# Kernel tuning notes

Hardware: AMD Instinct MI355X
Metric: run time of the kernel (lower is better)

The kernel has to match this reference:

```python
import jax, jax.numpy as jnp
import numpy as np

H = 128      # hidden_channels
FN = 6       # in_channels_node
FE = 3       # in_channels_edge
N = 40000    # nodes per chunk (pointnum)
E = 240000   # edges
C = 2        # per_t * batch_size chunks
S = 4        # n_mp_down[0] message-passing steps


def _ln(x, g, b, eps=1e-5):
    m = jnp.mean(x, axis=-1, keepdims=True)
    v = jnp.mean((x - m) ** 2, axis=-1, keepdims=True)
    return (x - m) * jax.lax.rsqrt(v + eps) * g + b


def setup_inputs() -> dict:
    key = jax.random.key(0)
    ks = iter(jax.random.split(key, 64))
    def W(*shape):
        fan_in = shape[-2]
        return jax.random.normal(next(ks), shape, jnp.float32) * (1.0 / np.sqrt(fan_in))
    z = lambda *s: jnp.zeros(s, jnp.float32)
    o = lambda *s: jnp.ones(s, jnp.float32)
    inp = {
        "x": jax.random.normal(next(ks), (C * N, FN), jnp.float32),
        "edge_attr": jax.random.normal(next(ks), (E, FE), jnp.float32),
        "mean_vec_x": jax.random.normal(next(ks), (FN,), jnp.float32) * 0.1,
        "std_vec_x": o(FN),
        "mean_vec_edge": jax.random.normal(next(ks), (FE,), jnp.float32) * 0.1,
        "std_vec_edge": o(FE),
        # node encoder: 3 linears + LayerNorm
        "nenc_w0": W(FN, H), "nenc_b0": z(H),
        "nenc_w1": W(H, H), "nenc_b1": z(H),
        "nenc_w2": W(H, H), "nenc_b2": z(H),
        "nenc_g": o(H), "nenc_be": z(H),
        # edge encoder: 3 linears + LayerNorm
        "eenc_w0": W(FE, H), "eenc_b0": z(H),
        "eenc_w1": W(H, H), "eenc_b1": z(H),
        "eenc_w2": W(H, H), "eenc_b2": z(H),
        "eenc_g": o(H), "eenc_be": z(H),
        # per-step edge MLPs (n_mlp_mp=2), stacked over S steps
        "emp_w0": W(S, 3 * H, H), "emp_b0": z(S, H),
        "emp_w1": W(S, H, H), "emp_b1": z(S, H),
        "emp_g": o(S, H), "emp_be": z(S, H),
        # per-step node MLPs
        "nmp_w0": W(S, 2 * H, H), "nmp_b0": z(S, H),
        "nmp_w1": W(S, H, H), "nmp_b1": z(S, H),
        "nmp_g": o(S, H), "nmp_be": z(S, H),
        "edge_index": jax.random.randint(next(ks), (2, E), 0, N, jnp.int32),
        "per_t": 2,
        "batch_size": 1,
    }
    return inp


def _forward(x, edge_attr, mean_vec_x, std_vec_x, mean_vec_edge, std_vec_edge,
             nenc_w0, nenc_b0, nenc_w1, nenc_b1, nenc_w2, nenc_b2, nenc_g, nenc_be,
             eenc_w0, eenc_b0, eenc_w1, eenc_b1, eenc_w2, eenc_b2, eenc_g, eenc_be,
             emp_w0, emp_b0, emp_w1, emp_b1, emp_g, emp_be,
             nmp_w0, nmp_b0, nmp_w1, nmp_b1, nmp_g, nmp_be,
             edge_index, per_t, batch_size):
    act = jax.nn.elu
    ei0, ei1 = edge_index[0], edge_index[1]
    chunks = per_t * batch_size
    n = x.shape[0] // chunks  # pointnum
    # edge encoding is identical for every chunk (shared edge_attr)
    e = (edge_attr - mean_vec_edge) / std_vec_edge
    e = act(e @ eenc_w0 + eenc_b0)
    e = act(e @ eenc_w1 + eenc_b1)
    e = e @ eenc_w2 + eenc_b2
    e0 = _ln(e, eenc_g, eenc_be)
    # scatter-mean denominator (PyG aggr='mean' at target nodes ei1)
    cnt = jax.ops.segment_sum(jnp.ones((ei1.shape[0], 1), x.dtype), ei1, num_segments=n)
    cnt = jnp.maximum(cnt, 1.0)

    def chunk(xc):  # xc: [n, FN]
        h = (xc - mean_vec_x) / std_vec_x
        h = act(h @ nenc_w0 + nenc_b0)
        h = act(h @ nenc_w1 + nenc_b1)
        h = h @ nenc_w2 + nenc_b2
        h = _ln(h, nenc_g, nenc_be)
        e = e0
        for s in range(S):
            # per-edge: gather -> concat -> 2-layer MLP -> residual -> LN
            et = jnp.concatenate([h[ei0], h[ei1], e], axis=-1)  # [E, 3H]
            et = act(et @ emp_w0[s] + emp_b0[s]) @ emp_w1[s] + emp_b1[s]
            e = _ln(e + et, emp_g[s], emp_be[s])
            # scatter-mean of edge features to target nodes
            agg = jax.ops.segment_sum(e, ei1, num_segments=n) / cnt  # [n, H]
            # per-node: concat -> 2-layer MLP -> residual -> LN
            ht = jnp.concatenate([h, agg], axis=-1)  # [n, 2H]
            ht = act(ht @ nmp_w0[s] + nmp_b0[s]) @ nmp_w1[s] + nmp_b1[s]
            h = _ln(h + ht, nmp_g[s], nmp_be[s])
        return h

    return jax.vmap(chunk)(x.reshape(chunks, n, FN))  # [C, n, H]


def reference(x, edge_attr, mean_vec_x, std_vec_x, mean_vec_edge, std_vec_edge,
              nenc_w0, nenc_b0, nenc_w1, nenc_b1, nenc_w2, nenc_b2, nenc_g, nenc_be,
              eenc_w0, eenc_b0, eenc_w1, eenc_b1, eenc_w2, eenc_b2, eenc_g, eenc_be,
              emp_w0, emp_b0, emp_w1, emp_b1, emp_g, emp_be,
              nmp_w0, nmp_b0, nmp_w1, nmp_b1, nmp_g, nmp_be,
              edge_index, per_t, batch_size):
    return _forward(x, edge_attr, mean_vec_x, std_vec_x, mean_vec_edge, std_vec_edge,
                    nenc_w0, nenc_b0, nenc_w1, nenc_b1, nenc_w2, nenc_b2, nenc_g, nenc_be,
                    eenc_w0, eenc_b0, eenc_w1, eenc_b1, eenc_w2, eenc_b2, eenc_g, eenc_be,
                    emp_w0, emp_b0, emp_w1, emp_b1, emp_g, emp_be,
                    nmp_w0, nmp_b0, nmp_w1, nmp_b1, nmp_g, nmp_be,
                    edge_index, per_t, batch_size)
```

## Files before the change

### kernel.cpp

```cpp
#include <hip/hip_runtime.h>
#include <math.h>

constexpr int HD  = 128;
constexpr int FNN = 6;
constexpr int FEE = 3;
constexpr int NN  = 40000;
constexpr int EE  = 240000;
constexpr int SS  = 4;

typedef __bf16 bf16_t;
typedef bf16_t bf16x8 __attribute__((ext_vector_type(8)));
typedef float  f32x4  __attribute__((ext_vector_type(4)));

__device__ __forceinline__ f32x4 mfma16(bf16x8 a, bf16x8 b, f32x4 c){
  return __builtin_amdgcn_mfma_f32_16x16x32_bf16(a, b, c, 0, 0, 0);
}
__device__ __forceinline__ float elu(float v){ return v > 0.f ? v : __expf(v) - 1.f; }

struct PackJob { const float* src; int K; };
struct PackArgs { PackJob j[30]; };

__global__ void __launch_bounds__(256) k_pack(PackArgs pa, bf16_t* __restrict__ dst){
  int gid = blockIdx.x*256 + threadIdx.x;
  int base = 0;
  #pragma unroll 1
  for (int i = 0; i < 30; ++i){
    int Kp = (pa.j[i].K + 31) & ~31;
    int sz = Kp * HD;
    if (gid < base + sz){
      int idx = gid - base;
      int jj = idx & 7, c = (idx >> 3) & 127, G = idx >> 10;
      int k = G*8 + jj;
      float v = (k < pa.j[i].K) ? pa.j[i].src[(size_t)k*HD + c] : 0.f;
      dst[base + idx] = (bf16_t)v;
      return;
    }
    base += sz;
  }
}

__global__ void k_cnt(const int* __restrict__ ei1, int* __restrict__ cnt){
  int t = blockIdx.x*blockDim.x + threadIdx.x;
  if (t < EE) atomicAdd(cnt + ei1[t], 1);
}

__global__ void __launch_bounds__(1024) k_scan(const int* __restrict__ cnt,
    int* __restrict__ rowstart, int* __restrict__ cursor, float* __restrict__ inv){
  __shared__ int sdata[1024];
  __shared__ int carry_s;
  if (threadIdx.x == 0) carry_s = 0;
  __syncthreads();
  for (int base = 0; base < NN; base += 1024){
    int i = base + (int)threadIdx.x;
    int orig = (i < NN) ? cnt[i] : 0;
    sdata[threadIdx.x] = orig;
    __syncthreads();
    #pragma unroll
    for (int ofs = 1; ofs < 1024; ofs <<= 1){
      int t = (threadIdx.x >= (unsigned)ofs) ? sdata[threadIdx.x - ofs] : 0;
      __syncthreads();
      sdata[threadIdx.x] += t;
      __syncthreads();
    }
    int incl = sdata[threadIdx.x];
    int carry = carry_s;
    if (i < NN){
      int start = carry + incl - orig;
      rowstart[i] = start;
      cursor[i]   = start;
      inv[i] = 1.f / fmaxf((float)orig, 1.f);
    }
    __syncthreads();
    if (threadIdx.x == 1023) carry_s = carry + incl;
    __syncthreads();
  }
  if (threadIdx.x == 0) rowstart[NN] = carry_s;
}

__global__ void k_fill(const int* __restrict__ ei0, const int* __restrict__ ei1,
                       int* __restrict__ cursor, int* __restrict__ perm,
                       int2* __restrict__ eidx2){
  int t = blockIdx.x*blockDim.x + threadIdx.x;
  if (t < EE){
    int n1 = ei1[t];
    int pos = atomicAdd(cursor + n1, 1);
    perm[pos] = t;
    int2 v; v.x = ei0[t]; v.y = n1;
    eidx2[pos] = v;
  }
}

__global__ void __launch_bounds__(256) k_agg(const bf16_t* __restrict__ e,
    const int* __restrict__ rowstart, const float* __restrict__ inv,
    bf16_t* __restrict__ agg){
  int gid = blockIdx.x*256 + (int)threadIdx.x;
  int node = gid >> 4, li = gid & 15;
  if (node >= NN) return;
  int s = rowstart[node], t = rowstart[node+1];
  float a[8] = {0,0,0,0,0,0,0,0};
  for (int ed = s; ed < t; ++ed){
    bf16x8 v = *(const bf16x8*)(e + (size_t)ed*HD + li*8);
    #pragma unroll
    for (int i = 0; i < 8; ++i) a[i] += (float)v[i];
  }
  float sc = inv[node];
  bf16x8 o;
  #pragma unroll
  for (int i = 0; i < 8; ++i) o[i] = (bf16_t)(a[i]*sc);
  *(bf16x8*)(agg + (size_t)node*HD + li*8) = o;
}

template<int FIN, bool ISNODE>
__global__ void __launch_bounds__(256) k_encoder(
    const float* __restrict__ xin, const float* __restrict__ mv, const float* __restrict__ sv,
    const float* __restrict__ w0,  const float* __restrict__ b0,
    const bf16_t* __restrict__ W1p, const float* __restrict__ b1,
    const bf16_t* __restrict__ W2p, const float* __restrict__ b2,
    const float* __restrict__ gg,  const float* __restrict__ bb,
    float* __restrict__ outf, bf16_t* __restrict__ outb,
    const int* __restrict__ perm)
{
  __shared__ bf16_t z0s[4][16][136];
  __shared__ bf16_t z1s[4][16][136];
  const int tid = threadIdx.x;
  const int w = tid >> 6, l = tid & 63, r = l & 15, grp = l >> 4;
  const int rowbase = blockIdx.x*64 + w*16;
  const int row = rowbase + r;
  const int src = perm ? perm[row] : row;

  float xn[FIN];
  #pragma unroll
  for (int f = 0; f < FIN; ++f) xn[f] = (xin[(size_t)src*FIN + f] - mv[f]) / sv[f];
  #pragma unroll
  for (int q = 0; q < 32; ++q){
    int c = grp*32 + q;
    float a = b0[c];
    #pragma unroll
    for (int f = 0; f < FIN; ++f) a += xn[f] * w0[f*HD + c];
    z0s[w][r][c] = (bf16_t)elu(a);
  }
  __syncthreads();

  bf16x8 a1[4];
  #pragma unroll
  for (int kt = 0; kt < 4; ++kt) a1[kt] = *(const bf16x8*)&z0s[w][r][kt*32 + grp*8];
  #pragma unroll
  for (int nt = 0; nt < 8; ++nt){
    int c = nt*16 + r;
    float bv = b1[c];
    f32x4 acc = {bv, bv, bv, bv};
    #pragma unroll
    for (int kt = 0; kt < 4; ++kt){
      bf16x8 bfr = *(const bf16x8*)(W1p + ((kt*4 + grp)*HD + c)*8);
      acc = mfma16(a1[kt], bfr, acc);
    }
    #pragma unroll
    for (int i = 0; i < 4; ++i) z1s[w][grp*4 + i][c] = (bf16_t)elu(acc[i]);
  }
  __syncthreads();

  bf16x8 a2[4];
  #pragma unroll
  for (int kt = 0; kt < 4; ++kt) a2[kt] = *(const bf16x8*)&z1s[w][r][kt*32 + grp*8];
  f32x4 et[8];
  #pragma unroll
  for (int nt = 0; nt < 8; ++nt){
    int c = nt*16 + r;
    float bv = b2[c];
    f32x4 acc = {bv, bv, bv, bv};
    #pragma unroll
    for (int kt = 0; kt < 4; ++kt){
      bf16x8 bfr = *(const bf16x8*)(W2p + ((kt*4 + grp)*HD + c)*8);
      acc = mfma16(a2[kt], bfr, acc);
    }
    et[nt] = acc;
  }

  f32x4 s = {0,0,0,0}, sq = {0,0,0,0};
  #pragma unroll
  for (int nt = 0; nt < 8; ++nt)
    #pragma unroll
    for (int i = 0; i < 4; ++i){ float v = et[nt][i]; s[i] += v; sq[i] += v*v; }
  #pragma unroll
  for (int m = 1; m < 16; m <<= 1)
    #pragma unroll
    for (int i = 0; i < 4; ++i){ s[i] += __shfl_xor(s[i], m, 64); sq[i] += __shfl_xor(sq[i], m, 64); }
  f32x4 mean, rstd;
  #pragma unroll
  for (int i = 0; i < 4; ++i){
    float mu = s[i] * (1.f/HD);
    float va = sq[i] * (1.f/HD) - mu*mu;
    mean[i] = mu; rstd[i] = rsqrtf(va + 1e-5f);
  }
  #pragma unroll
  for (int nt = 0; nt < 8; ++nt){
    int c = nt*16 + r;
    float gv = gg[c], bv = bb[c];
    #pragma unroll
    for (int i = 0; i < 4; ++i){
      float o = (et[nt][i] - mean[i]) * rstd[i] * gv + bv;
      size_t oidx = (size_t)(rowbase + grp*4 + i)*HD + c;
      outb[oidx] = (bf16_t)o;
      if constexpr (ISNODE) outf[oidx] = o;
    }
  }
}

__global__ void __launch_bounds__(256) k_hpartial(
    const bf16_t* __restrict__ hbf,
    const bf16_t* __restrict__ Wap, const bf16_t* __restrict__ Wbp,
    bf16_t* __restrict__ p0, bf16_t* __restrict__ p1)
{
  const int tid = threadIdx.x;
  const int w = tid >> 6, l = tid & 63, r = l & 15, grp = l >> 4;
  const int rowbase = blockIdx.x*64 + w*16;
  const int row = rowbase + r;

  bf16x8 afr[4];
  #pragma unroll
  for (int kt = 0; kt < 4; ++kt)
    afr[kt] = *(const bf16x8*)(hbf + (size_t)row*HD + kt*32 + grp*8);

  #pragma unroll
  for (int nt = 0; nt < 8; ++nt){
    int c = nt*16 + r;
    f32x4 a0 = {0,0,0,0}, a1 = {0,0,0,0};
    #pragma unroll
    for (int kt = 0; kt < 4; ++kt){
      bf16x8 bfa = *(const bf16x8*)(Wap + ((kt*4 + grp)*HD + c)*8);
      bf16x8 bfb = *(const bf16x8*)(Wbp + ((kt*4 + grp)*HD + c)*8);
      a0 = mfma16(afr[kt], bfa, a0);
      a1 = mfma16(afr[kt], bfb, a1);
    }
    #pragma unroll
    for (int i = 0; i < 4; ++i){
      size_t oidx = (size_t)(rowbase + grp*4 + i)*HD + c;
      p0[oidx] = (bf16_t)a0[i];
      p1[oidx] = (bf16_t)a1[i];
    }
  }
}

__global__ void __launch_bounds__(256) k_edge_mlp(
    const bf16_t* __restrict__ p0g, const bf16_t* __restrict__ p1g,
    const bf16_t* e_in, bf16_t* e_out,
    const bf16_t* __restrict__ W0ep, const float* __restrict__ b0,
    const bf16_t* __restrict__ W1p, const float* __restrict__ b1,
    const float* __restrict__ gg,  const float* __restrict__ bb,
    const int2* __restrict__ eidx2)
{
  __shared__ bf16_t z1s_all[4][16][136];
  const int tid = threadIdx.x;
  const int w = tid >> 6, l = tid & 63, r = l & 15, grp = l >> 4;
  const int rowbase = blockIdx.x*64 + w*16;
  const int row = rowbase + r;
  bf16_t (*z1)[136] = z1s_all[w];

  {
    const int sr = l >> 2, cq = (l & 3)*32;
    const int2 nnS = eidx2[rowbase + sr];
    const bf16_t* P0 = p0g + (size_t)nnS.x*HD + cq;
    const bf16_t* P1 = p1g + (size_t)nnS.y*HD + cq;
    #pragma unroll
    for (int q = 0; q < 4; ++q){
      bf16x8 u = *(const bf16x8*)(P0 + q*8);
      bf16x8 v = *(const bf16x8*)(P1 + q*8);
      bf16x8 sm;
      #pragma unroll
      for (int i = 0; i < 8; ++i) sm[i] = (bf16_t)((float)u[i] + (float)v[i]);
      *(bf16x8*)&z1[sr][cq + q*8] = sm;
    }
  }

  bf16x8 afr[4];
  #pragma unroll
  for (int kt = 0; kt < 4; ++kt)
    afr[kt] = *(const bf16x8*)(e_in + (size_t)row*HD + kt*32 + grp*8);
  __builtin_amdgcn_wave_barrier();

  #pragma unroll
  for (int nt = 0; nt < 8; ++nt){
    int c = nt*16 + r;
    float bv = b0[c];
    f32x4 acc = {bv, bv, bv, bv};
    #pragma unroll
    for (int kt = 0; kt < 4; ++kt){
      bf16x8 bfr = *(const bf16x8*)(W0ep + ((kt*4 + grp)*HD + c)*8);
      acc = mfma16(afr[kt], bfr, acc);
    }
    #pragma unroll
    for (int i = 0; i < 4; ++i){
      float pv = (float)z1[grp*4 + i][c];
      z1[grp*4 + i][c] = (bf16_t)elu(acc[i] + pv);
    }
  }
  __builtin_amdgcn_wave_barrier();

  bf16x8 a2[4];
  #pragma unroll
  for (int kt = 0; kt < 4; ++kt) a2[kt] = *(const bf16x8*)&z1[r][kt*32 + grp*8];
  f32x4 et[8];
  #pragma unroll
  for (int nt = 0; nt < 8; ++nt){
    int c = nt*16 + r;
    float bv = b1[c];
    f32x4 acc = {bv, bv, bv, bv};
    #pragma unroll
    for (int kt = 0; kt < 4; ++kt){
      bf16x8 bfr = *(const bf16x8*)(W1p + ((kt*4 + grp)*HD + c)*8);
      acc = mfma16(a2[kt], bfr, acc);
    }
    et[nt] = acc;
  }

  f32x4 s = {0,0,0,0}, sq = {0,0,0,0};
  #pragma unroll
  for (int nt = 0; nt < 8; ++nt){
    int c = nt*16 + r;
    #pragma unroll
    for (int i = 0; i < 4; ++i){
      float v = et[nt][i] + (float)e_in[(size_t)(rowbase + grp*4 + i)*HD + c];
      et[nt][i] = v; s[i] += v; sq[i] += v*v;
    }
  }
  #pragma unroll
  for (int m = 1; m < 16; m <<= 1)
    #pragma unroll
    for (int i = 0; i < 4; ++i){ s[i] += __shfl_xor(s[i], m, 64); sq[i] += __shfl_xor(sq[i], m, 64); }
  f32x4 mean, rstd;
  #pragma unroll
  for (int i = 0; i < 4; ++i){
    float mu = s[i] * (1.f/HD);
    float va = sq[i] * (1.f/HD) - mu*mu;
    mean[i] = mu; rstd[i] = rsqrtf(va + 1e-5f);
  }
  #pragma unroll
  for (int nt = 0; nt < 8; ++nt){
    int c = nt*16 + r;
    float gv = gg[c], bv = bb[c];
    #pragma unroll
    for (int i = 0; i < 4; ++i)
      e_out[(size_t)(rowbase + grp*4 + i)*HD + c] =
          (bf16_t)((et[nt][i] - mean[i]) * rstd[i] * gv + bv);
  }
}

__global__ void __launch_bounds__(256) k_node_mlp(
    bf16_t* hbf, const bf16_t* __restrict__ agg,
    const bf16_t* __restrict__ W0p, const float* __restrict__ b0,
    const bf16_t* __restrict__ W1p, const float* __restrict__ b1,
    const float* __restrict__ gg,  const float* __restrict__ bb,
    float* hout)
{
  __shared__ bf16_t z1s[4][16][136];
  const int tid = threadIdx.x;
  const int w = tid >> 6, l = tid & 63, r = l & 15, grp = l >> 4;
  const int rowbase = blockIdx.x*64 + w*16;
  const int row = rowbase + r;

  bf16x8 afr[8];
  #pragma unroll
  for (int kt = 0; kt < 4; ++kt)
    afr[kt] = *(const bf16x8*)(hbf + (size_t)row*HD + kt*32 + grp*8);
  #pragma unroll
  for (int kt = 0; kt < 4; ++kt)
    afr[4+kt] = *(const bf16x8*)(agg + (size_t)row*HD + kt*32 + grp*8);

  #pragma unroll
  for (int nt = 0; nt < 8; ++nt){
    int c = nt*16 + r;
    float bv = b0[c];
    f32x4 acc = {bv, bv, bv, bv};
    #pragma unroll
    for (int kt = 0; kt < 8; ++kt){
      bf16x8 bfr = *(const bf16x8*)(W0p + ((kt*4 + grp)*HD + c)*8);
      acc = mfma16(afr[kt], bfr, acc);
    }
    #pragma unroll
    for (int i = 0; i < 4; ++i) z1s[w][grp*4 + i][c] = (bf16_t)elu(acc[i]);
  }
  __syncthreads();

  bf16x8 a2[4];
  #pragma unroll
  for (int kt = 0; kt < 4; ++kt) a2[kt] = *(const bf16x8*)&z1s[w][r][kt*32 + grp*8];
  f32x4 et[8];
  #pragma unroll
  for (int nt = 0; nt < 8; ++nt){
    int c = nt*16 + r;
    float bv = b1[c];
    f32x4 acc = {bv, bv, bv, bv};
    #pragma unroll
    for (int kt = 0; kt < 4; ++kt){
      bf16x8 bfr = *(const bf16x8*)(W1p + ((kt*4 + grp)*HD + c)*8);
      acc = mfma16(a2[kt], bfr, acc);
    }
    et[nt] = acc;
  }

  f32x4 s = {0,0,0,0}, sq = {0,0,0,0};
  #pragma unroll
  for (int nt = 0; nt < 8; ++nt){
    int c = nt*16 + r;
    #pragma unroll
    for (int i = 0; i < 4; ++i){
      float v = et[nt][i] + hout[(size_t)(rowbase + grp*4 + i)*HD + c];
      et[nt][i] = v; s[i] += v; sq[i] += v*v;
    }
  }
  #pragma unroll
  for (int m = 1; m < 16; m <<= 1)
    #pragma unroll
    for (int i = 0; i < 4; ++i){ s[i] += __shfl_xor(s[i], m, 64); sq[i] += __shfl_xor(sq[i], m, 64); }
  f32x4 mean, rstd;
  #pragma unroll
  for (int i = 0; i < 4; ++i){
    float mu = s[i] * (1.f/HD);
    float va = sq[i] * (1.f/HD) - mu*mu;
    mean[i] = mu; rstd[i] = rsqrtf(va + 1e-5f);
  }
  #pragma unroll
  for (int nt = 0; nt < 8; ++nt){
    int c = nt*16 + r;
    float gv = gg[c], bv = bb[c];
    #pragma unroll
    for (int i = 0; i < 4; ++i){
      float o = (et[nt][i] - mean[i]) * rstd[i] * gv + bv;
      size_t oidx = (size_t)(rowbase + grp*4 + i)*HD + c;
      hout[oidx] = o;
      hbf[oidx]  = (bf16_t)o;
    }
  }
}

extern "C" void kernel_launch(void* const* d_in, const int* in_sizes, int n_in,
                              void* d_out, int out_size, void* d_ws, size_t ws_size,
                              hipStream_t stream)
{
  (void)in_sizes; (void)n_in; (void)out_size; (void)ws_size;
  const float* x         = (const float*)d_in[0];
  const float* edge_attr = (const float*)d_in[1];
  const float* mvx = (const float*)d_in[2];
  const float* svx = (const float*)d_in[3];
  const float* mve = (const float*)d_in[4];
  const float* sve = (const float*)d_in[5];
  const float* nenc_w0 = (const float*)d_in[6];
  const float* nenc_b0 = (const float*)d_in[7];
  const float* nenc_w1 = (const float*)d_in[8];
  const float* nenc_b1 = (const float*)d_in[9];
  const float* nenc_w2 = (const float*)d_in[10];
  const float* nenc_b2 = (const float*)d_in[11];
  const float* nenc_g  = (const float*)d_in[12];
  const float* nenc_be = (const float*)d_in[13];
  const float* eenc_w0 = (const float*)d_in[14];
  const float* eenc_b0 = (const float*)d_in[15];
  const float* eenc_w1 = (const float*)d_in[16];
  const float* eenc_b1 = (const float*)d_in[17];
  const float* eenc_w2 = (const float*)d_in[18];
  const float* eenc_b2 = (const float*)d_in[19];
  const float* eenc_g  = (const float*)d_in[20];
  const float* eenc_be = (const float*)d_in[21];
  const float* emp_w0 = (const float*)d_in[22];
  const float* emp_b0 = (const float*)d_in[23];
  const float* emp_w1 = (const float*)d_in[24];
  const float* emp_b1 = (const float*)d_in[25];
  const float* emp_g  = (const float*)d_in[26];
  const float* emp_be = (const float*)d_in[27];
  const float* nmp_w0 = (const float*)d_in[28];
  const float* nmp_b0 = (const float*)d_in[29];
  const float* nmp_w1 = (const float*)d_in[30];
  const float* nmp_b1 = (const float*)d_in[31];
  const float* nmp_g  = (const float*)d_in[32];
  const float* nmp_be = (const float*)d_in[33];
  const int* eidx = (const int*)d_in[34];
  const int* ei0 = eidx;
  const int* ei1 = eidx + EE;
  float* out = (float*)d_out;

  char* ws = (char*)d_ws;
  size_t off = 0;
  bf16_t* e_cur = (bf16_t*)(ws + off); off += (size_t)EE*HD*2;
  bf16_t* e0    = (bf16_t*)(ws + off); off += (size_t)EE*HD*2;
  bf16_t* hbf   = (bf16_t*)(ws + off); off += (size_t)NN*HD*2;
  bf16_t* agg   = (bf16_t*)(ws + off); size_t agg_off = off; off += (size_t)NN*HD*2;
  bf16_t* p0    = (bf16_t*)(ws + off); off += (size_t)NN*HD*2;
  bf16_t* p1    = (bf16_t*)(ws + off); off += (size_t)NN*HD*2;
  float*  inv   = (float*)(ws + off);  off += (size_t)NN*4;
  int*    rowst = (int*)(ws + off);    off += (size_t)(NN+1)*4 + 12;
  int*    perm  = (int*)(ws + off);    off += (size_t)EE*4;
  int2*   eidx2 = (int2*)(ws + off);   off += (size_t)EE*8;
  bf16_t* wpk   = (bf16_t*)(ws + off);
  int*    cnt_i = (int*)(ws + agg_off);
  int*    curs  = (int*)(ws + agg_off + (size_t)NN*4);

  hipMemsetAsync(cnt_i, 0, NN*sizeof(int), stream);
  k_cnt<<<(EE + 255)/256, 256, 0, stream>>>(ei1, cnt_i);
  k_scan<<<1, 1024, 0, stream>>>(cnt_i, rowst, curs, inv);
  k_fill<<<(EE + 255)/256, 256, 0, stream>>>(ei0, ei1, curs, perm, eidx2);

  PackArgs pa;
  const float* srcs[30] = {
    eenc_w0, eenc_w1, eenc_w2, nenc_w0, nenc_w1, nenc_w2,
    emp_w0,           emp_w0 + 49152,           emp_w0 + 2*49152,           emp_w0 + 3*49152,
    emp_w0 + 16384,   emp_w0 + 49152 + 16384,   emp_w0 + 2*49152 + 16384,   emp_w0 + 3*49152 + 16384,
    emp_w0 + 32768,   emp_w0 + 49152 + 32768,   emp_w0 + 2*49152 + 32768,   emp_w0 + 3*49152 + 32768,
    emp_w1, emp_w1 + 16384, emp_w1 + 2*16384, emp_w1 + 3*16384,
    nmp_w0, nmp_w0 + 32768, nmp_w0 + 2*32768, nmp_w0 + 3*32768,
    nmp_w1, nmp_w1 + 16384, nmp_w1 + 2*16384, nmp_w1 + 3*16384 };
  const int KsA[30] = {FEE,128,128,FNN,128,128,
                       128,128,128,128, 128,128,128,128, 128,128,128,128,
                       128,128,128,128, 256,256,256,256, 128,128,128,128};
  int offs[30]; int tot = 0;
  for (int i = 0; i < 30; ++i){
    pa.j[i].src = srcs[i]; pa.j[i].K = KsA[i];
    offs[i] = tot; tot += ((KsA[i] + 31) & ~31) * HD;
  }
  k_pack<<<(tot + 255)/256, 256, 0, stream>>>(pa, wpk);

  k_encoder<FEE,false><<<EE/64, 256, 0, stream>>>(edge_attr, mve, sve,
      eenc_w0, eenc_b0, wpk + offs[1], eenc_b1, wpk + offs[2], eenc_b2,
      eenc_g, eenc_be, nullptr, e0, perm);

  for (int c = 0; c < 2; ++c){
    float* hout = out + (size_t)c*NN*HD;
    k_encoder<FNN,true><<<NN/64, 256, 0, stream>>>(x + (size_t)c*NN*FNN, mvx, svx,
        nenc_w0, nenc_b0, wpk + offs[4], nenc_b1, wpk + offs[5], nenc_b2,
        nenc_g, nenc_be, hout, hbf, nullptr);
    for (int s = 0; s < SS; ++s){
      const bf16_t* e_in = (s == 0) ? e0 : e_cur;
      k_hpartial<<<NN/64, 256, 0, stream>>>(hbf,
          wpk + offs[6+s], wpk + offs[10+s], p0, p1);
      k_edge_mlp<<<EE/64, 256, 0, stream>>>(p0, p1, e_in, e_cur,
          wpk + offs[14+s], emp_b0 + s*HD, wpk + offs[18+s], emp_b1 + s*HD,
          emp_g + s*HD, emp_be + s*HD, eidx2);
      k_agg<<<(NN*16 + 255)/256, 256, 0, stream>>>(e_cur, rowst, inv, agg);
      k_node_mlp<<<NN/64, 256, 0, stream>>>(hbf, agg,
          wpk + offs[22+s], nmp_b0 + s*HD, wpk + offs[26+s], nmp_b1 + s*HD,
          nmp_g + s*HD, nmp_be + s*HD, hout);
    }
  }
}
```

Before: 1.145 ms.

## Fuse next-step node partial projections into node MLP; parallelize CSR scan

The per-step k_hpartial launch, which reread hbf to compute the two node-side projections for the edge MLP, is folded into the tail of k_node_mlp. The freshly normalized rows are staged in shared memory and multiplied there by the next step's weights, removing one launch and one full read of hbf per step. The single-block serial scan over node counts is replaced by a three-kernel multi-block scan (block scan, block offsets, apply) to shorten the setup phase. In exchange the node MLP kernel does more work per block and needs more registers, and the setup path adds two extra launches.

New measurement: 1.082 ms. 1.06x faster.

```diff
diff --git a/kernel.cpp b/kernel.cpp
--- a/kernel.cpp
+++ b/kernel.cpp
@@ -44,37 +44,42 @@
   if (t < EE) atomicAdd(cnt + ei1[t], 1);
 }
 
-__global__ void __launch_bounds__(1024) k_scan(const int* __restrict__ cnt,
+__global__ void __launch_bounds__(1024) k_scanA(const int* __restrict__ cnt,
+    int* __restrict__ incl, int* __restrict__ bsum){
+  __shared__ int sd[1024];
+  int i = blockIdx.x*1024 + (int)threadIdx.x;
+  int v = (i < NN) ? cnt[i] : 0;
+  sd[threadIdx.x] = v;
+  __syncthreads();
+  #pragma unroll
+  for (int ofs = 1; ofs < 1024; ofs <<= 1){
+    int t = (threadIdx.x >= (unsigned)ofs) ? sd[threadIdx.x - ofs] : 0;
+    __syncthreads();
+    sd[threadIdx.x] += t;
+    __syncthreads();
+  }
+  if (i < NN) incl[i] = sd[threadIdx.x];
+  if (threadIdx.x == 1023) bsum[blockIdx.x] = sd[1023];
+}
+__global__ void k_scanB(const int* __restrict__ bsum, int* __restrict__ boff, int nb){
+  if (threadIdx.x == 0){
+    int acc = 0;
+    for (int b = 0; b < nb; ++b){ boff[b] = acc; acc += bsum[b]; }
+    boff[nb] = acc;
+  }
+}
+__global__ void __launch_bounds__(1024) k_scanC(const int* __restrict__ cnt,
+    const int* __restrict__ incl, const int* __restrict__ boff,
     int* __restrict__ rowstart, int* __restrict__ cursor, float* __restrict__ inv){
-  __shared__ int sdata[1024];
-  __shared__ int carry_s;
-  if (threadIdx.x == 0) carry_s = 0;
-  __syncthreads();
-  for (int base = 0; base < NN; base += 1024){
-    int i = base + (int)threadIdx.x;
-    int orig = (i < NN) ? cnt[i] : 0;
-    sdata[threadIdx.x] = orig;
-    __syncthreads();
-    #pragma unroll
-    for (int ofs = 1; ofs < 1024; ofs <<= 1){
-      int t = (threadIdx.x >= (unsigned)ofs) ? sdata[threadIdx.x - ofs] : 0;
-      __syncthreads();
-      sdata[threadIdx.x] += t;
-      __syncthreads();
-    }
-    int incl = sdata[threadIdx.x];
-    int carry = carry_s;
-    if (i < NN){
-      int start = carry + incl - orig;
-      rowstart[i] = start;
-      cursor[i]   = start;
-      inv[i] = 1.f / fmaxf((float)orig, 1.f);
-    }
-    __syncthreads();
-    if (threadIdx.x == 1023) carry_s = carry + incl;
-    __syncthreads();
-  }
-  if (threadIdx.x == 0) rowstart[NN] = carry_s;
+  int i = blockIdx.x*1024 + (int)threadIdx.x;
+  if (i < NN){
+    int c = cnt[i];
+    int start = boff[blockIdx.x] + incl[i] - c;
+    rowstart[i] = start;
+    cursor[i]   = start;
+    inv[i] = 1.f / fmaxf((float)c, 1.f);
+  }
+  if (blockIdx.x == 0 && threadIdx.x == 0) rowstart[NN] = boff[gridDim.x];
 }
 
 __global__ void k_fill(const int* __restrict__ ei0, const int* __restrict__ ei1,
@@ -345,12 +350,15 @@
   }
 }
 
+template<bool DOPART>
 __global__ void __launch_bounds__(256) k_node_mlp(
     bf16_t* hbf, const bf16_t* __restrict__ agg,
     const bf16_t* __restrict__ W0p, const float* __restrict__ b0,
     const bf16_t* __restrict__ W1p, const float* __restrict__ b1,
     const float* __restrict__ gg,  const float* __restrict__ bb,
-    float* hout)
+    float* hout,
+    const bf16_t* __restrict__ Wap, const bf16_t* __restrict__ Wbp,
+    bf16_t* __restrict__ p0, bf16_t* __restrict__ p1)
 {
   __shared__ bf16_t z1s[4][16][136];
   const int tid = threadIdx.x;
@@ -427,8 +435,35 @@
     for (int i = 0; i < 4; ++i){
       float o = (et[nt][i] - mean[i]) * rstd[i] * gv + bv;
       size_t oidx = (size_t)(rowbase + grp*4 + i)*HD + c;
+      bf16_t ob = (bf16_t)o;
       hout[oidx] = o;
-      hbf[oidx]  = (bf16_t)o;
+      hbf[oidx]  = ob;
+      if constexpr (DOPART) z1s[w][grp*4 + i][c] = ob;
+    }
+  }
+
+  if constexpr (DOPART){
+    __builtin_amdgcn_wave_barrier();
+    bf16x8 ah[4];
+    #pragma unroll
+    for (int kt = 0; kt < 4; ++kt) ah[kt] = *(const bf16x8*)&z1s[w][r][kt*32 + grp*8];
+    #pragma unroll
+    for (int nt = 0; nt < 8; ++nt){
+      int c = nt*16 + r;
+      f32x4 a0 = {0,0,0,0}, a1 = {0,0,0,0};
+      #pragma unroll
+      for (int kt = 0; kt < 4; ++kt){
+        bf16x8 bfa = *(const bf16x8*)(Wap + ((kt*4 + grp)*HD + c)*8);
+        bf16x8 bfb = *(const bf16x8*)(Wbp + ((kt*4 + grp)*HD + c)*8);
+        a0 = mfma16(ah[kt], bfa, a0);
+        a1 = mfma16(ah[kt], bfb, a1);
+      }
+      #pragma unroll
+      for (int i = 0; i < 4; ++i){
+        size_t oidx = (size_t)(rowbase + grp*4 + i)*HD + c;
+        p0[oidx] = (bf16_t)a0[i];
+        p1[oidx] = (bf16_t)a1[i];
+      }
     }
   }
 }
@@ -492,10 +527,17 @@
   bf16_t* wpk   = (bf16_t*)(ws + off);
   int*    cnt_i = (int*)(ws + agg_off);
   int*    curs  = (int*)(ws + agg_off + (size_t)NN*4);
+  int*    incl  = (int*)(ws + agg_off + (size_t)2*NN*4);
+  int*    bsum  = (int*)(ws + agg_off + (size_t)3*NN*4);
+  int*    boff  = (int*)(ws + agg_off + (size_t)3*NN*4 + 256);
+
+  const int NB = (NN + 1023)/1024;
 
   hipMemsetAsync(cnt_i, 0, NN*sizeof(int), stream);
   k_cnt<<<(EE + 255)/256, 256, 0, stream>>>(ei1, cnt_i);
-  k_scan<<<1, 1024, 0, stream>>>(cnt_i, rowst, curs, inv);
+  k_scanA<<<NB, 1024, 0, stream>>>(cnt_i, incl, bsum);
+  k_scanB<<<1, 64, 0, stream>>>(bsum, boff, NB);
+  k_scanC<<<NB, 1024, 0, stream>>>(cnt_i, incl, boff, rowst, curs, inv);
   k_fill<<<(EE + 255)/256, 256, 0, stream>>>(ei0, ei1, curs, perm, eidx2);
 
   PackArgs pa;
@@ -526,17 +568,24 @@
     k_encoder<FNN,true><<<NN/64, 256, 0, stream>>>(x + (size_t)c*NN*FNN, mvx, svx,
         nenc_w0, nenc_b0, wpk + offs[4], nenc_b1, wpk + offs[5], nenc_b2,
         nenc_g, nenc_be, hout, hbf, nullptr);
+    k_hpartial<<<NN/64, 256, 0, stream>>>(hbf, wpk + offs[6], wpk + offs[10], p0, p1);
     for (int s = 0; s < SS; ++s){
       const bf16_t* e_in = (s == 0) ? e0 : e_cur;
-      k_hpartial<<<NN/64, 256, 0, stream>>>(hbf,
-          wpk + offs[6+s], wpk + offs[10+s], p0, p1);
       k_edge_mlp<<<EE/64, 256, 0, stream>>>(p0, p1, e_in, e_cur,
           wpk + offs[14+s], emp_b0 + s*HD, wpk + offs[18+s], emp_b1 + s*HD,
           emp_g + s*HD, emp_be + s*HD, eidx2);
       k_agg<<<(NN*16 + 255)/256, 256, 0, stream>>>(e_cur, rowst, inv, agg);
-      k_node_mlp<<<NN/64, 256, 0, stream>>>(hbf, agg,
-          wpk + offs[22+s], nmp_b0 + s*HD, wpk + offs[26+s], nmp_b1 + s*HD,
-          nmp_g + s*HD, nmp_be + s*HD, hout);
-    }
-  }
-}
+      if (s < SS-1){
+        k_node_mlp<true><<<NN/64, 256, 0, stream>>>(hbf, agg,
+            wpk + offs[22+s], nmp_b0 + s*HD, wpk + offs[26+s], nmp_b1 + s*HD,
+            nmp_g + s*HD, nmp_be + s*HD, hout,
+            wpk + offs[6+(s+1)], wpk + offs[10+(s+1)], p0, p1);
+      } else {
+        k_node_mlp<false><<<NN/64, 256, 0, stream>>>(hbf, agg,
+            wpk + offs[22+s], nmp_b0 + s*HD, wpk + offs[26+s], nmp_b1 + s*HD,
+            nmp_g + s*HD, nmp_be + s*HD, hout,
+            nullptr, nullptr, nullptr, nullptr);
+      }
+    }
+  }
+}
```
